# Kernel optimization log

Hardware: AMD Instinct MI355X
Metric: run time of the kernel (lower is better)

The kernel has to match this reference:

```python
import jax, jax.numpy as jnp
import numpy as np

# Architecture constants (match init_kwargs)
STEPS, BATCH = 256, 128
IN_SIZE, H1, H2, OUT = 512, 1536, 1536, 512
DELAY = 1


def setup_inputs() -> dict:
    key = jax.random.key(0)
    ks = jax.random.split(key, 5)
    def init_w(k, shape):
        fan_in = shape[0]
        return (jax.random.normal(k, shape, jnp.float32) / np.sqrt(fan_in).astype(np.float32))
    return {
        "inputs": jax.random.normal(ks[0], (STEPS, BATCH, IN_SIZE), jnp.float32),
        # hidden1 RNNC: in = sizes['#input'] + sizes['hidden1'] (self-recurrent conn)
        "W1": init_w(ks[1], (IN_SIZE + H1, H1)),
        "b1": jnp.zeros((H1,), jnp.float32),
        # hidden2 RNNC: in = sizes['hidden1'] + sizes['hidden2']
        "W2": init_w(ks[2], (H1 + H2, H2)),
        "b2": jnp.zeros((H2,), jnp.float32),
        # '##output' PlaceholderWt: linear readout from hidden2
        "Wo": init_w(ks[3], (H2, OUT)),
        "bo": jnp.zeros((OUT,), jnp.float32),
    }


def reference(inputs, W1, b1, W2, b2, Wo, bo):
    # Stepped multi-layer RNN with delay=1 spike buffers.
    # Within a step, layers update in order, so a layer reading spikes_all[-1]
    # of an EARLIER layer sees the current step's spike, while self/backward
    # connections see the previous step's spike (carried through the scan).
    B = inputs.shape[1]

    def step(carry, x_t):
        s_h1_prev, s_h2_prev = carry
        s_in = x_t                                               # Placeholder '#input'
        # hidden1: prevs = ['#input' (current), 'hidden1' (prev step)]
        s_h1 = jnp.tanh(jnp.concatenate([s_in, s_h1_prev], -1) @ W1 + b1)
        # hidden2: prevs = ['hidden1' (current), 'hidden2' (prev step)]
        s_h2 = jnp.tanh(jnp.concatenate([s_h1, s_h2_prev], -1) @ W2 + b2)
        # '##output' PlaceholderWt: linear readout of current hidden2 spike
        out = s_h2 @ Wo + bo
        return (s_h1, s_h2), out

    init = (jnp.zeros((B, H1), inputs.dtype), jnp.zeros((B, H2), inputs.dtype))
    _, outs = jax.lax.scan(step, init, inputs)                   # [steps, B, OUT]
    # spikes_all includes `delay` initial zero spikes from reset_state
    zeros = jnp.zeros((DELAY, B, OUT), inputs.dtype)
    return jnp.concatenate([zeros, outs], axis=0)                # [delay+steps, B, OUT]
```

## Files before the change

kernel.cpp:

```cpp
#include <hip/hip_runtime.h>
#include <math.h>

#define STEPS 256
#define BATCH 128
#define HALF_M 64
#define INSZ  512
#define H1SZ  1536
#define H2SZ  1536
#define NOUT  512
#define K1    2048
#define K2    3072
#define NC1   48
#define NC2   48
#define NC3   16
#define NBLK  224
#define RING  8

typedef short bf16x8 __attribute__((ext_vector_type(8)));
typedef float f32x4  __attribute__((ext_vector_type(4)));
typedef unsigned short u16;

__device__ __forceinline__ f32x4 mfma16(bf16x8 a, bf16x8 b, f32x4 c) {
  return __builtin_amdgcn_mfma_f32_16x16x32_bf16(a, b, c, 0, 0, 0);
}

__device__ __forceinline__ u16 f2bf(float f) {
  unsigned u = __builtin_bit_cast(unsigned, f);
  u += 0x7fffu + ((u >> 16) & 1u);
  return (u16)(u >> 16);
}

__device__ __forceinline__ bf16x8 cvt8(const float* p) {
  f32x4 lo = *(const f32x4*)p;
  f32x4 hi = *(const f32x4*)(p + 4);
  union { unsigned u[4]; bf16x8 v; } r;
  asm("v_cvt_pk_bf16_f32 %0, %1, %2" : "=v"(r.u[0]) : "v"(lo[0]), "v"(lo[1]));
  asm("v_cvt_pk_bf16_f32 %0, %1, %2" : "=v"(r.u[1]) : "v"(lo[2]), "v"(lo[3]));
  asm("v_cvt_pk_bf16_f32 %0, %1, %2" : "=v"(r.u[2]) : "v"(hi[0]), "v"(hi[1]));
  asm("v_cvt_pk_bf16_f32 %0, %1, %2" : "=v"(r.u[3]) : "v"(hi[2]), "v"(hi[3]));
  return r.v;
}

#define LOAD_SC_OFS(dst, ptr, ofs) \
  asm volatile("global_load_dwordx4 %0, %1, off offset:%2 sc0 sc1" \
               : "=v"(dst) : "v"(ptr), "i"(ofs) : "memory")
#define STORE_SC(ptr, val) \
  asm volatile("global_store_dwordx4 %0, %1, off sc0 sc1" :: "v"(ptr), "v"(val) : "memory")
#define WAITV(n) asm volatile("s_waitcnt vmcnt(" #n ")" ::: "memory")
#define PIN4(v)  asm volatile("" : "+v"(v))
#define PINA(v)  asm volatile("" : "+a"(v))
#define MFMA_AB(acc, va, ab) \
  asm volatile("v_mfma_f32_16x16x32_bf16 %0, %1, %2, %0" : "+v"(acc) : "v"(va), "a"(ab))
#define MFMA_FENCE() asm volatile("s_nop 7\n\ts_nop 7\n\ts_nop 7")

__device__ __forceinline__ void set_flag(int* p, int v) {
  __hip_atomic_store(p, v, __ATOMIC_RELAXED, __HIP_MEMORY_SCOPE_SYSTEM);
}

__device__ __forceinline__ void wave_wait(const int* p, int tgt, bool active) {
  while (true) {
    int v = __hip_atomic_load(p, __ATOMIC_RELAXED, __HIP_MEMORY_SCOPE_SYSTEM);
    if (!__any(active && (v < tgt))) break;
    __builtin_amdgcn_s_sleep(1);
  }
}

__device__ __forceinline__ void kloop12a(const u16* base, const bf16x8 (&Ba)[12][2],
                                         f32x4 (&acc)[4][2], int r16) {
  const u16* rp[4];
#pragma unroll
  for (int mf = 0; mf < 4; ++mf) rp[mf] = base + (size_t)(mf * 16 + r16) * 1536;
  bf16x8 A[12][4];
  WAITV(0);
#pragma unroll
  for (int d = 0; d < 12; ++d)
#pragma unroll
    for (int mf = 0; mf < 4; ++mf)
      LOAD_SC_OFS(A[d][mf], rp[mf], d * 64);
#pragma unroll
  for (int ks = 0; ks < 12; ++ks) {
    const int rem = 11 - ks;
    if (rem == 11)      WAITV(44);
    else if (rem == 10) WAITV(40);
    else if (rem == 9)  WAITV(36);
    else if (rem == 8)  WAITV(32);
    else if (rem == 7)  WAITV(28);
    else if (rem == 6)  WAITV(24);
    else if (rem == 5)  WAITV(20);
    else if (rem == 4)  WAITV(16);
    else if (rem == 3)  WAITV(12);
    else if (rem == 2)  WAITV(8);
    else if (rem == 1)  WAITV(4);
    else                WAITV(0);
    __builtin_amdgcn_sched_barrier(0);
#pragma unroll
    for (int mf = 0; mf < 4; ++mf) {
      MFMA_AB(acc[mf][0], A[ks][mf], Ba[ks][0]);
      MFMA_AB(acc[mf][1], A[ks][mf], Ba[ks][1]);
    }
  }
  MFMA_FENCE();
}

__device__ __forceinline__ void kloop_x4(const float* xb, const bf16x8 (&Br)[4][2],
                                         f32x4 (&acc)[4][2], int r16) {
#pragma unroll
  for (int ks = 0; ks < 4; ++ks)
#pragma unroll
    for (int mf = 0; mf < 4; ++mf) {
      bf16x8 a = cvt8(xb + (size_t)(mf * 16 + r16) * INSZ + ks * 32);
      acc[mf][0] = mfma16(a, Br[ks][0], acc[mf][0]);
      acc[mf][1] = mfma16(a, Br[ks][1], acc[mf][1]);
    }
}

__device__ __forceinline__ void store_red(float (*red)[64][36], int kw, int kg, int r16,
                                          const f32x4 (&acc)[4][2]) {
#pragma unroll
  for (int mf = 0; mf < 4; ++mf)
#pragma unroll
    for (int nf = 0; nf < 2; ++nf)
#pragma unroll
      for (int r = 0; r < 4; ++r)
        red[kw][mf * 16 + kg * 4 + r][nf * 16 + r16] = acc[mf][nf][r];
}

__device__ __forceinline__ void epi_tanh(const float (*red)[64][36], f32x4 bv0, f32x4 bv1,
                                         u16* dstbase, int n0, int tid) {
  const int row = tid >> 2, c0 = (tid & 3) * 8;
  f32x4 s0 = bv0, s1 = bv1;
#pragma unroll
  for (int w = 0; w < 4; ++w) {
    s0 += *(const f32x4*)&red[w][row][c0];
    s1 += *(const f32x4*)&red[w][row][c0 + 4];
  }
  float t[8];
#pragma unroll
  for (int j = 0; j < 4; ++j) t[j] = tanhf(s0[j]);
#pragma unroll
  for (int j = 0; j < 4; ++j) t[4 + j] = tanhf(s1[j]);
  union { unsigned u[4]; bf16x8 v; } pk;
  asm("v_cvt_pk_bf16_f32 %0, %1, %2" : "=v"(pk.u[0]) : "v"(t[0]), "v"(t[1]));
  asm("v_cvt_pk_bf16_f32 %0, %1, %2" : "=v"(pk.u[1]) : "v"(t[2]), "v"(t[3]));
  asm("v_cvt_pk_bf16_f32 %0, %1, %2" : "=v"(pk.u[2]) : "v"(t[4]), "v"(t[5]));
  asm("v_cvt_pk_bf16_f32 %0, %1, %2" : "=v"(pk.u[3]) : "v"(t[6]), "v"(t[7]));
  u16* dst = dstbase + (size_t)row * 1536 + n0 + c0;
  STORE_SC(dst, pk.v);
}

__global__ __launch_bounds__(256)
__attribute__((amdgpu_waves_per_eu(1, 1)))
void rnn_main(
    const float* __restrict__ x,
    const u16* __restrict__ W1T, const u16* __restrict__ W2T, const u16* __restrict__ WoT,
    const float* __restrict__ b1, const float* __restrict__ b2, const float* __restrict__ bo,
    u16* __restrict__ h1ring, u16* __restrict__ h2ring,
    float* __restrict__ out, int* __restrict__ bar)
{
  __shared__ float red[4][64][36];
  const int tid = threadIdx.x;
  const int kw = tid >> 6, lane = tid & 63;
  const int r16 = lane & 15, kg = lane >> 4;
  const int bid = blockIdx.x;

  int grp, half, col;
  if (bid < 2 * NC1)              { grp = 0; half = bid / NC1;         col = bid % NC1; }
  else if (bid < 2 * (NC1 + NC2)) { grp = 1; half = (bid - 96) / NC2;  col = (bid - 96) % NC2; }
  else                            { grp = 2; half = (bid - 192) / NC3; col = (bid - 192) % NC3; }
  const int n0 = col * 32;
  int* f1 = bar + (half * NC1) * 16;
  int* f2 = bar + (96 + half * NC2) * 16;
  int* f3 = bar + (192 + half * NC3) * 16;

  u16* h1base = h1ring + (size_t)half * RING * HALF_M * H1SZ;
  u16* h2base = h2ring + (size_t)half * RING * HALF_M * H2SZ;

  const int* wpA = f1; int dA = 0; bool aA = false;
  const int* wpB = f1; int dB = 0; bool aB = false;
  if (grp == 0) {
    if (lane < 12)                  { wpA = f1 + (kw * 12 + lane) * 16; dA = 0;  aA = true; }
    else if (kw == 0 && lane >= 16) { wpA = f2 + (lane - 16) * 16;      dA = -6; aA = true; }
  } else if (grp == 1) {
    if (lane < 12) {
      wpA = f2 + (kw * 12 + lane) * 16; dA = 0; aA = true;
      wpB = f1 + (kw * 12 + lane) * 16; dB = 1; aB = true;
    } else if (kw == 0 && lane >= 32 && lane < 48) {
      wpA = f3 + (lane - 32) * 16; dA = -6; aA = true;
    }
  } else {
    if (lane < 12)                  { wpA = f2 + (kw * 12 + lane) * 16; dA = 1;  aA = true; }
  }

  if (grp == 0) {
    bf16x8 BrX[4][2], Brh[12][2];
#pragma unroll
    for (int ks = 0; ks < 4; ++ks)
#pragma unroll
      for (int nf = 0; nf < 2; ++nf)
        BrX[ks][nf] = *(const bf16x8*)(W1T + (size_t)(n0 + nf * 16 + r16) * K1
                                       + kw * 128 + ks * 32 + kg * 8);
#pragma unroll
    for (int ks = 0; ks < 12; ++ks)
#pragma unroll
      for (int nf = 0; nf < 2; ++nf)
        Brh[ks][nf] = *(const bf16x8*)(W1T + (size_t)(n0 + nf * 16 + r16) * K1
                                       + 512 + kw * 384 + ks * 32 + kg * 8);
#pragma unroll
    for (int ks = 0; ks < 4; ++ks) { PIN4(BrX[ks][0]); PIN4(BrX[ks][1]); }
#pragma unroll
    for (int ks = 0; ks < 12; ++ks) { PINA(Brh[ks][0]); PINA(Brh[ks][1]); }
    asm volatile("s_nop 7\n\ts_nop 7");
    const f32x4 bv0 = *(const f32x4*)(b1 + n0 + (tid & 3) * 8);
    const f32x4 bv1 = *(const f32x4*)(b1 + n0 + (tid & 3) * 8 + 4);

    for (int k = 0; k < STEPS; ++k) {
      f32x4 acc[4][2] = {};
      const float* xb = x + ((size_t)k * BATCH + half * HALF_M) * INSZ + kw * 128 + kg * 8;
      kloop_x4(xb, BrX, acc, r16);
      wave_wait(wpA, k + dA, aA);
      kloop12a(h1base + (size_t)((k + RING - 1) & (RING - 1)) * HALF_M * H1SZ
               + kw * 384 + kg * 8, Brh, acc, r16);
      store_red(red, kw, kg, r16, acc);
      __syncthreads();
      epi_tanh(red, bv0, bv1, h1base + (size_t)(k & (RING - 1)) * HALF_M * H1SZ, n0, tid);
      WAITV(0);
      __syncthreads();
      if (tid == 0) set_flag(&f1[col * 16], k + 1);
    }
  } else if (grp == 1) {
    bf16x8 Bh2[12][2], Bh1[12][2];
#pragma unroll
    for (int ks = 0; ks < 12; ++ks)
#pragma unroll
      for (int nf = 0; nf < 2; ++nf) {
        Bh2[ks][nf] = *(const bf16x8*)(W2T + (size_t)(n0 + nf * 16 + r16) * K2
                                       + 1536 + kw * 384 + ks * 32 + kg * 8);
        Bh1[ks][nf] = *(const bf16x8*)(W2T + (size_t)(n0 + nf * 16 + r16) * K2
                                       + kw * 384 + ks * 32 + kg * 8);
      }
#pragma unroll
    for (int ks = 0; ks < 12; ++ks) { PINA(Bh2[ks][0]); PINA(Bh2[ks][1]);
                                      PINA(Bh1[ks][0]); PINA(Bh1[ks][1]); }
    asm volatile("s_nop 7\n\ts_nop 7");
    const f32x4 bv0 = *(const f32x4*)(b2 + n0 + (tid & 3) * 8);
    const f32x4 bv1 = *(const f32x4*)(b2 + n0 + (tid & 3) * 8 + 4);

    for (int j = 0; j < STEPS; ++j) {
      f32x4 acc[4][2] = {};
      wave_wait(wpA, j + dA, aA);
      kloop12a(h2base + (size_t)((j + RING - 1) & (RING - 1)) * HALF_M * H2SZ
               + kw * 384 + kg * 8, Bh2, acc, r16);
      wave_wait(wpB, j + dB, aB);
      kloop12a(h1base + (size_t)(j & (RING - 1)) * HALF_M * H1SZ
               + kw * 384 + kg * 8, Bh1, acc, r16);
      store_red(red, kw, kg, r16, acc);
      __syncthreads();
      epi_tanh(red, bv0, bv1, h2base + (size_t)(j & (RING - 1)) * HALF_M * H2SZ, n0, tid);
      WAITV(0);
      __syncthreads();
      if (tid == 0) set_flag(&f2[col * 16], j + 1);
    }
  } else {
    bf16x8 Br[12][2];
#pragma unroll
    for (int ks = 0; ks < 12; ++ks)
#pragma unroll
      for (int nf = 0; nf < 2; ++nf)
        Br[ks][nf] = *(const bf16x8*)(WoT + (size_t)(n0 + nf * 16 + r16) * H2SZ
                                      + kw * 384 + ks * 32 + kg * 8);
#pragma unroll
    for (int ks = 0; ks < 12; ++ks) { PINA(Br[ks][0]); PINA(Br[ks][1]); }
    asm volatile("s_nop 7\n\ts_nop 7");
    const f32x4 bv0 = *(const f32x4*)(bo + n0 + (tid & 3) * 8);
    const f32x4 bv1 = *(const f32x4*)(bo + n0 + (tid & 3) * 8 + 4);

    for (int j = 0; j < STEPS; ++j) {
      f32x4 acc[4][2] = {};
      wave_wait(wpA, j + dA, aA);
      kloop12a(h2base + (size_t)(j & (RING - 1)) * HALF_M * H2SZ
               + kw * 384 + kg * 8, Br, acc, r16);
      store_red(red, kw, kg, r16, acc);
      __syncthreads();
      {
        const int row = tid >> 2, c0 = (tid & 3) * 8;
        f32x4 s0 = bv0, s1 = bv1;
#pragma unroll
        for (int w = 0; w < 4; ++w) {
          s0 += *(const f32x4*)&red[w][row][c0];
          s1 += *(const f32x4*)&red[w][row][c0 + 4];
        }
        float* dst = out + ((size_t)(j + 1) * BATCH + half * HALF_M + row) * NOUT + n0 + c0;
        *(f32x4*)dst = s0;
        *(f32x4*)(dst + 4) = s1;
      }
      __syncthreads();
      if (tid == 0) set_flag(&f3[col * 16], j + 1);
    }
  }
}

__global__ void transpose_cvt(const float* __restrict__ src, u16* __restrict__ dst, int K, int N) {
  __shared__ u16 tile[32][33];
  int kb = blockIdx.x * 32, nb = blockIdx.y * 32;
  int tx = threadIdx.x & 31, ty = threadIdx.x >> 5;
  for (int i = ty; i < 32; i += 8)
    tile[i][tx] = f2bf(src[(size_t)(kb + i) * N + nb + tx]);
  __syncthreads();
  for (int i = ty; i < 32; i += 8)
    dst[(size_t)(nb + i) * K + kb + tx] = tile[tx][i];
}

extern "C" void kernel_launch(void* const* d_in, const int* in_sizes, int n_in,
                              void* d_out, int out_size, void* d_ws, size_t ws_size,
                              hipStream_t stream) {
  const float* x  = (const float*)d_in[0];
  const float* W1 = (const float*)d_in[1];
  const float* b1 = (const float*)d_in[2];
  const float* W2 = (const float*)d_in[3];
  const float* b2 = (const float*)d_in[4];
  const float* Wo = (const float*)d_in[5];
  const float* bo = (const float*)d_in[6];
  float* out = (float*)d_out;
  char*  ws  = (char*)d_ws;

  u16* W1T    = (u16*)(ws);
  u16* W2T    = (u16*)(ws + 6291456);
  u16* WoT    = (u16*)(ws + 15728640);
  u16* h1ring = (u16*)(ws + 17301504);
  u16* h2ring = (u16*)(ws + 20447232);
  int* bar    = (int*)(ws + 23592960);

  hipMemsetAsync(ws + 17301504, 0, 3145728 * 2 + 14336, stream);
  hipMemsetAsync(d_out, 0, (size_t)BATCH * NOUT * sizeof(float), stream);

  transpose_cvt<<<dim3(K1 / 32, H1SZ / 32), 256, 0, stream>>>(W1, W1T, K1, H1SZ);
  transpose_cvt<<<dim3(K2 / 32, H1SZ / 32), 256, 0, stream>>>(W2, W2T, K2, H1SZ);
  transpose_cvt<<<dim3(H2SZ / 32, NOUT / 32), 256, 0, stream>>>(Wo, WoT, H2SZ, NOUT);

  rnn_main<<<NBLK, 256, 0, stream>>>(x, W1T, W2T, WoT, b1, b2, bo, h1ring, h2ring, out, bar);
}
```

Measured before the change: 3.407 ms.

## Replace cache-bypassing sc loads with acquire fence and plain cached loads

Each block now acquires once (a block barrier plus an agent-scope acquire load by one thread) after the flag waits and then uses ordinary cached vector loads for the hidden-state tiles. This replaces the per-load sc0 sc1 system-coherent loads with their hand-written vmcnt pipeline. Layer 2 now waits for both dependencies up front and reads the h1 tile before the h2 tile, which gives up the overlap of the earlier wait-then-load ordering. The output stores become sc stores followed by a wait. The intent is to let hidden-state reads hit L2 instead of bypassing it, at the cost of extra block barriers and a weaker, compiler-scheduled load pipeline.

```diff
diff --git a/kernel.cpp b/kernel.cpp
--- a/kernel.cpp
+++ b/kernel.cpp
@@ -41,9 +41,6 @@
   return r.v;
 }
 
-#define LOAD_SC_OFS(dst, ptr, ofs) \
-  asm volatile("global_load_dwordx4 %0, %1, off offset:%2 sc0 sc1" \
-               : "=v"(dst) : "v"(ptr), "i"(ofs) : "memory")
 #define STORE_SC(ptr, val) \
   asm volatile("global_store_dwordx4 %0, %1, off sc0 sc1" :: "v"(ptr), "v"(val) : "memory")
 #define WAITV(n) asm volatile("s_waitcnt vmcnt(" #n ")" ::: "memory")
@@ -65,40 +62,21 @@
   }
 }
 
-__device__ __forceinline__ void kloop12a(const u16* base, const bf16x8 (&Ba)[12][2],
+__device__ __forceinline__ void acq_fence(const int* p) {
+  int v = __hip_atomic_load(p, __ATOMIC_ACQUIRE, __HIP_MEMORY_SCOPE_AGENT);
+  asm volatile("" :: "v"(v));
+}
+
+__device__ __forceinline__ void kloop12p(const u16* base, const bf16x8 (&Ba)[12][2],
                                          f32x4 (&acc)[4][2], int r16) {
-  const u16* rp[4];
-#pragma unroll
-  for (int mf = 0; mf < 4; ++mf) rp[mf] = base + (size_t)(mf * 16 + r16) * 1536;
-  bf16x8 A[12][4];
-  WAITV(0);
-#pragma unroll
-  for (int d = 0; d < 12; ++d)
-#pragma unroll
-    for (int mf = 0; mf < 4; ++mf)
-      LOAD_SC_OFS(A[d][mf], rp[mf], d * 64);
-#pragma unroll
-  for (int ks = 0; ks < 12; ++ks) {
-    const int rem = 11 - ks;
-    if (rem == 11)      WAITV(44);
-    else if (rem == 10) WAITV(40);
-    else if (rem == 9)  WAITV(36);
-    else if (rem == 8)  WAITV(32);
-    else if (rem == 7)  WAITV(28);
-    else if (rem == 6)  WAITV(24);
-    else if (rem == 5)  WAITV(20);
-    else if (rem == 4)  WAITV(16);
-    else if (rem == 3)  WAITV(12);
-    else if (rem == 2)  WAITV(8);
-    else if (rem == 1)  WAITV(4);
-    else                WAITV(0);
-    __builtin_amdgcn_sched_barrier(0);
+#pragma unroll
+  for (int ks = 0; ks < 12; ++ks)
 #pragma unroll
     for (int mf = 0; mf < 4; ++mf) {
-      MFMA_AB(acc[mf][0], A[ks][mf], Ba[ks][0]);
-      MFMA_AB(acc[mf][1], A[ks][mf], Ba[ks][1]);
-    }
-  }
+      bf16x8 a = *(const bf16x8*)(base + (size_t)(mf * 16 + r16) * 1536 + ks * 32);
+      MFMA_AB(acc[mf][0], a, Ba[ks][0]);
+      MFMA_AB(acc[mf][1], a, Ba[ks][1]);
+    }
   MFMA_FENCE();
 }
 
@@ -218,7 +196,10 @@
       const float* xb = x + ((size_t)k * BATCH + half * HALF_M) * INSZ + kw * 128 + kg * 8;
       kloop_x4(xb, BrX, acc, r16);
       wave_wait(wpA, k + dA, aA);
-      kloop12a(h1base + (size_t)((k + RING - 1) & (RING - 1)) * HALF_M * H1SZ
+      __syncthreads();
+      if (tid == 0) acq_fence(f1);
+      __syncthreads();
+      kloop12p(h1base + (size_t)((k + RING - 1) & (RING - 1)) * HALF_M * H1SZ
                + kw * 384 + kg * 8, Brh, acc, r16);
       store_red(red, kw, kg, r16, acc);
       __syncthreads();
@@ -246,13 +227,16 @@
     const f32x4 bv1 = *(const f32x4*)(b2 + n0 + (tid & 3) * 8 + 4);
 
     for (int j = 0; j < STEPS; ++j) {
+      wave_wait(wpB, j + dB, aB);
+      wave_wait(wpA, j + dA, aA);
+      __syncthreads();
+      if (tid == 0) acq_fence(f2);
+      __syncthreads();
       f32x4 acc[4][2] = {};
-      wave_wait(wpA, j + dA, aA);
-      kloop12a(h2base + (size_t)((j + RING - 1) & (RING - 1)) * HALF_M * H2SZ
+      kloop12p(h1base + (size_t)(j & (RING - 1)) * HALF_M * H1SZ
+               + kw * 384 + kg * 8, Bh1, acc, r16);
+      kloop12p(h2base + (size_t)((j + RING - 1) & (RING - 1)) * HALF_M * H2SZ
                + kw * 384 + kg * 8, Bh2, acc, r16);
-      wave_wait(wpB, j + dB, aB);
-      kloop12a(h1base + (size_t)(j & (RING - 1)) * HALF_M * H1SZ
-               + kw * 384 + kg * 8, Bh1, acc, r16);
       store_red(red, kw, kg, r16, acc);
       __syncthreads();
       epi_tanh(red, bv0, bv1, h2base + (size_t)(j & (RING - 1)) * HALF_M * H2SZ, n0, tid);
@@ -275,9 +259,12 @@
     const f32x4 bv1 = *(const f32x4*)(bo + n0 + (tid & 3) * 8 + 4);
 
     for (int j = 0; j < STEPS; ++j) {
+      wave_wait(wpA, j + dA, aA);
+      __syncthreads();
+      if (tid == 0) acq_fence(f2);
+      __syncthreads();
       f32x4 acc[4][2] = {};
-      wave_wait(wpA, j + dA, aA);
-      kloop12a(h2base + (size_t)(j & (RING - 1)) * HALF_M * H2SZ
+      kloop12p(h2base + (size_t)(j & (RING - 1)) * HALF_M * H2SZ
                + kw * 384 + kg * 8, Br, acc, r16);
       store_red(red, kw, kg, r16, acc);
       __syncthreads();
@@ -290,9 +277,10 @@
           s1 += *(const f32x4*)&red[w][row][c0 + 4];
         }
         float* dst = out + ((size_t)(j + 1) * BATCH + half * HALF_M + row) * NOUT + n0 + c0;
-        *(f32x4*)dst = s0;
-        *(f32x4*)(dst + 4) = s1;
+        STORE_SC(dst, s0);
+        STORE_SC((dst + 4), s1);
       }
+      WAITV(0);
       __syncthreads();
       if (tid == 0) set_flag(&f3[col * 16], j + 1);
     }
```

New measurement: 4.504 ms. +32.2%, slower.
